# Kernel tuning notes

Measured on AMD Instinct MI355X. Metric: run time of the kernel, lower is better.

The kernel has to match this reference:

```python
import jax, jax.numpy as jnp
import numpy as np
import math

N, E, MUL = 10000, 160000, 128
D = MUL * 4  # 128x0e (128) + 128x1o (384) = 512
NEURONS = 32
EDGE_ATTR_DIM = 32
WEIGHT_NUMEL = 4 * MUL  # 4 uvu tensor-product paths, 128 weights each


def ssp(x):
    return jax.nn.softplus(x) - math.log(2.0)


def irrep_linear(x, W0, b0, W1):
    # o3.Linear on 128x0e+128x1o: mixes mul channels within each irrep, fan-in normalized,
    # bias only on scalar (0e) block.
    s = x[:, :MUL] @ (W0 / jnp.sqrt(MUL)) + b0
    v = x[:, MUL:].reshape(-1, MUL, 3)
    v = jnp.einsum('num,uv->nvm', v, W1) / jnp.sqrt(MUL)
    return jnp.concatenate([s, v.reshape(-1, MUL * 3)], axis=-1)


def inner_product(a, b):
    # InnerProduct: uuu channel-wise irrep inner product, 1/sqrt(dim) normalized
    s = a[:, :MUL] * b[:, :MUL]
    va = a[:, MUL:].reshape(-1, MUL, 3)
    vb = b[:, MUL:].reshape(-1, MUL, 3)
    v = jnp.einsum('num,num->nu', va, vb) / jnp.sqrt(3.0)
    return jnp.concatenate([s, v], axis=-1)


def norm_gate(x, W1, b1, W2, b2):
    # NormGate: per-channel norms of l>0 irreps -> MLP gates -> gate l>0 channels
    v = x[:, MUL:].reshape(-1, MUL, 3)
    norm_v = jnp.sqrt(jnp.sum(v * v, axis=-1) + 1e-12)      # [n, 128]
    f0 = jnp.concatenate([x[:, :MUL], norm_v], axis=-1)     # [n, 256]
    g = jax.nn.silu(f0 @ W1 + b1) @ W2 + b2                 # [n, 256]
    gated = v * g[:, MUL:, None]
    return jnp.concatenate([g[:, :MUL], gated.reshape(-1, MUL * 3)], axis=-1)


def mlp2(x, Wa, Wb):
    # e3nn FullyConnectedNet: fan-in normalized, ssp nonlinearity on hidden layer only
    return ssp(x @ (Wa / jnp.sqrt(Wa.shape[0]))) @ (Wb / jnp.sqrt(Wb.shape[0]))


def setup_inputs():
    key = jax.random.key(0)
    ks = jax.random.split(key, 20)
    r = lambda i, shp: jax.random.normal(ks[i], shp, dtype=jnp.float32)
    return {
        'x': r(0, (N, D)),
        'edge_index': jax.random.randint(ks[1], (2, E), 0, N, dtype=jnp.int32),
        'edge_attr': jax.random.uniform(ks[2], (E, EDGE_ATTR_DIM), dtype=jnp.float32),
        'edge_sh': r(3, (E, 4)),
        'Wp0': r(4, (MUL, MUL)), 'bp0': jnp.zeros((MUL,), jnp.float32), 'Wp1': r(5, (MUL, MUL)),
        'ngW1': r(6, (2 * MUL, 2 * MUL)) / 16.0, 'ngb1': jnp.zeros((2 * MUL,), jnp.float32),
        'ngW2': r(7, (2 * MUL, 2 * MUL)) / 16.0, 'ngb2': jnp.zeros((2 * MUL,), jnp.float32),
        'Wn0': r(8, (MUL, MUL)), 'bn0': jnp.zeros((MUL,), jnp.float32), 'Wn1': r(9, (MUL, MUL)),
        'fcnW1': r(10, (EDGE_ATTR_DIM, NEURONS)), 'fcnW2': r(11, (NEURONS, WEIGHT_NUMEL)),
        'l0W1': r(12, (3 * MUL, NEURONS)), 'l0W2': r(13, (NEURONS, WEIGHT_NUMEL)),
        'Wo0': r(14, (MUL, MUL)), 'bo0': jnp.zeros((MUL,), jnp.float32), 'Wo1': r(15, (MUL, MUL)),
    }


def reference(x, edge_index, edge_attr, edge_sh, Wp0, bp0, Wp1, ngW1, ngb1, ngW2, ngb2,
              Wn0, bn0, Wn1, fcnW1, fcnW2, l0W1, l0W2, Wo0, bo0, Wo1):
    edge_dst, edge_src = edge_index[0], edge_index[1]
    # invariant edge descriptor s0 from pre-linear + inner product
    pre_x = irrep_linear(x, Wp0, bp0, Wp1)
    ip = inner_product(pre_x[edge_dst], pre_x[edge_src])[:, MUL:]             # [E,128]
    s0 = jnp.concatenate([pre_x[edge_dst][:, :MUL], pre_x[edge_src][:, :MUL], ip], axis=-1)  # [E,384]
    # norm-gate + linear on node features
    x = norm_gate(x, ngW1, ngb1, ngW2, ngb2)
    x = irrep_linear(x, Wn0, bn0, Wn1)
    self_x = x
    # per-edge tensor-product weights: fc_node(edge_attr) * layer_l0(s0)
    w = mlp2(edge_attr, fcnW1, fcnW2) * mlp2(s0, l0W1, l0W2)                   # [E,512]
    w1, w2, w3, w4 = w[:, :MUL], w[:, MUL:2 * MUL], w[:, 2 * MUL:3 * MUL], w[:, 3 * MUL:]
    xs = x[edge_src]
    xs0 = xs[:, :MUL]                     # [E,128]
    xs1 = xs[:, MUL:].reshape(E, MUL, 3)  # [E,128,3]
    sh0 = edge_sh[:, 0:1]
    sh1 = edge_sh[:, 1:4]
    # uvu CG tensor product paths: 0ex0e->0e, 0ex1o->1o, 1ox0e->1o, 1ox1o->0e
    c0, c1 = 0.5, jnp.sqrt(3.0) / 2.0  # path norm sqrt(ir_out.dim / n_paths)
    out0 = c0 * (w1 * xs0 * sh0 + w4 * jnp.einsum('eum,em->eu', xs1, sh1) / jnp.sqrt(3.0))
    out1 = c1 * (w2[:, :, None] * xs0[:, :, None] * sh1[:, None, :]
                 + w3[:, :, None] * xs1 * sh0[:, :, None])
    edge_feat = jnp.concatenate([out0, out1.reshape(E, MUL * 3)], axis=-1)     # [E,512]
    # scatter-aggregate to destination nodes, residual, output linear
    out = jax.ops.segment_sum(edge_feat, edge_dst, num_segments=N)
    out = out + self_x
    return irrep_linear(out, Wo0, bo0, Wo1)
```

## Files before the change

### kernel.cpp

```cpp
#include <hip/hip_runtime.h>
#include <hip/hip_fp16.h>
#include <math.h>

#define NN 10000
#define EE 160000
#define DPB 8

#define RS128 0.08838834764831845f
#define RS384 0.05103103630798287f
#define RS32  0.17677669529663687f
#define R3    0.57735026918962576f
#define C1V   0.86602540378443865f

typedef _Float16 half8 __attribute__((ext_vector_type(8)));
typedef float f32x4 __attribute__((ext_vector_type(4)));

__device__ __forceinline__ float sspf(float x) {
    return fmaxf(x, 0.0f) + log1pf(__expf(-fabsf(x))) - 0.69314718055994530942f;
}

__device__ __forceinline__ void packone(const float* __restrict__ W,
                                        _Float16* __restrict__ P,
                                        int K, int N, int off) {
    const int KS = K >> 5;
    int j = off & 7, lane = (off >> 3) & 63, rest = off >> 9;
    int ks = rest % KS, ct = rest / KS;
    int k = ks * 32 + ((lane >> 4) << 3) + j;
    int c = ct * 16 + (lane & 15);
    P[off] = (_Float16)W[k * N + c];
}

__global__ __launch_bounds__(256) void k_packall(
    const float* __restrict__ Wp0, const float* __restrict__ Wp1,
    const float* __restrict__ Wn0, const float* __restrict__ Wn1,
    const float* __restrict__ Wo0, const float* __restrict__ Wo1,
    const float* __restrict__ ngW1, const float* __restrict__ ngW2,
    const float* __restrict__ l0W1, const float* __restrict__ fcnW1,
    const float* __restrict__ fcnW2, const float* __restrict__ l0W2,
    _Float16* __restrict__ pWp0, _Float16* __restrict__ pWp1,
    _Float16* __restrict__ pWn0, _Float16* __restrict__ pWn1,
    _Float16* __restrict__ pWo0, _Float16* __restrict__ pWo1,
    _Float16* __restrict__ png1, _Float16* __restrict__ png2,
    _Float16* __restrict__ pWc, _Float16* __restrict__ pWa,
    _Float16* __restrict__ Wf_t, _Float16* __restrict__ Wl_t) {
    int idx = blockIdx.x * 256 + threadIdx.x;
    if (idx < 98304) {
        int seg = idx >> 14, off = idx & 16383;
        if (seg == 0) packone(Wp0, pWp0, 128, 128, off);
        else if (seg == 1) packone(Wp1, pWp1, 128, 128, off);
        else if (seg == 2) packone(Wn0, pWn0, 128, 128, off);
        else if (seg == 3) packone(Wn1, pWn1, 128, 128, off);
        else if (seg == 4) packone(Wo0, pWo0, 128, 128, off);
        else packone(Wo1, pWo1, 128, 128, off);
    } else if (idx < 229376) {
        int r = idx - 98304;
        if (r < 65536) packone(ngW1, png1, 256, 256, r);
        else packone(ngW2, png2, 256, 256, r - 65536);
    } else if (idx < 233472) {
        packone(l0W1 + 256 * 32, pWc, 128, 32, idx - 229376);
    } else if (idx < 234496) {
        packone(fcnW1, pWa, 32, 32, idx - 233472);
    } else {
        int off = idx - 234496;
        int k = off & 31, c = off >> 5;
        Wf_t[c * 32 + k] = (_Float16)fcnW2[k * 512 + c];
        Wl_t[c * 32 + k] = (_Float16)l0W2[k * 512 + c];
    }
}

__global__ __launch_bounds__(256) void k_irrep_m(
    const float* __restrict__ X, const _Float16* __restrict__ pW0,
    const float* __restrict__ b0, const _Float16* __restrict__ pW1,
    float* __restrict__ out) {
    __shared__ _Float16 Xr[4][16][136];
    const int t = threadIdx.x, lane = t & 63, w = t >> 6;
    const int nb = blockIdx.x * 16;
    for (int idx = t; idx < 16 * 128; idx += 256) {
        int n = idx >> 7, c4 = idx & 127;
        const float4 v = *(const float4*)(X + (size_t)(nb + n) * 512 + 4 * c4);
        float vals[4] = {v.x, v.y, v.z, v.w};
        int c = 4 * c4;
#pragma unroll
        for (int j = 0; j < 4; ++j) {
            int cc = c + j;
            if (cc < 128) Xr[0][n][cc] = (_Float16)vals[j];
            else { int d = cc - 128; Xr[1 + d % 3][n][d / 3] = (_Float16)vals[j]; }
        }
    }
    __syncthreads();
    const _Float16* pW = (w == 0) ? pW0 : pW1;
    const int row16 = lane & 15, kg = lane >> 4;
    f32x4 acc[8];
    const f32x4 zero = {0.0f, 0.0f, 0.0f, 0.0f};
#pragma unroll
    for (int ct = 0; ct < 8; ++ct) acc[ct] = zero;
    for (int ks = 0; ks < 4; ++ks) {
        const half8 a = *(const half8*)&Xr[w][row16][ks * 32 + kg * 8];
#pragma unroll
        for (int ct = 0; ct < 8; ++ct) {
            const half8 b = *(const half8*)(pW + (((ct * 4 + ks) * 64 + lane) << 3));
            acc[ct] = __builtin_amdgcn_mfma_f32_16x16x32_f16(a, b, acc[ct], 0, 0, 0);
        }
    }
#pragma unroll
    for (int ct = 0; ct < 8; ++ct) {
        const int col = ct * 16 + row16;
        const float bb = (w == 0) ? b0[col] : 0.0f;
#pragma unroll
        for (int r = 0; r < 4; ++r) {
            const int node = nb + kg * 4 + r;
            const float val = acc[ct][r] * RS128 + bb;
            if (w == 0) out[(size_t)node * 512 + col] = val;
            else out[(size_t)node * 512 + 128 + 3 * col + (w - 1)] = val;
        }
    }
}

__global__ __launch_bounds__(256) void k_self_m(
    const float* __restrict__ X,
    const _Float16* __restrict__ png1, const float* __restrict__ ngb1,
    const _Float16* __restrict__ png2, const float* __restrict__ ngb2,
    const _Float16* __restrict__ pWn0, const float* __restrict__ bn0,
    const _Float16* __restrict__ pWn1,
    float* __restrict__ selfx) {
    __shared__ _Float16 f0h[16][264];
    __shared__ _Float16 t1h[16][264];
    __shared__ _Float16 xvh[3][16][136];
    const int t = threadIdx.x, lane = t & 63, w = t >> 6;
    const int nb = blockIdx.x * 16;
    const int row16 = lane & 15, kg = lane >> 4;
    const f32x4 zero = {0.0f, 0.0f, 0.0f, 0.0f};

    for (int idx = t; idx < 16 * 128; idx += 256) {
        int n = idx >> 7, c4 = idx & 127;
        const float4 v = *(const float4*)(X + (size_t)(nb + n) * 512 + 4 * c4);
        float vals[4] = {v.x, v.y, v.z, v.w};
        int c = 4 * c4;
#pragma unroll
        for (int j = 0; j < 4; ++j) {
            int cc = c + j;
            if (cc < 128) f0h[n][cc] = (_Float16)vals[j];
            else { int d = cc - 128; xvh[d % 3][n][d / 3] = (_Float16)vals[j]; }
        }
    }
    __syncthreads();
    for (int idx = t; idx < 16 * 128; idx += 256) {
        int n = idx >> 7, u = idx & 127;
        float a = (float)xvh[0][n][u], b = (float)xvh[1][n][u], c = (float)xvh[2][n][u];
        f0h[n][128 + u] = (_Float16)sqrtf(fmaf(a, a, fmaf(b, b, fmaf(c, c, 1e-12f))));
    }
    __syncthreads();
    {
        f32x4 acc[4];
#pragma unroll
        for (int i = 0; i < 4; ++i) acc[i] = zero;
        for (int ks = 0; ks < 8; ++ks) {
            const half8 a = *(const half8*)&f0h[row16][ks * 32 + kg * 8];
#pragma unroll
            for (int c2 = 0; c2 < 4; ++c2) {
                const int ct = 4 * w + c2;
                const half8 b = *(const half8*)(png1 + (((ct * 8 + ks) * 64 + lane) << 3));
                acc[c2] = __builtin_amdgcn_mfma_f32_16x16x32_f16(a, b, acc[c2], 0, 0, 0);
            }
        }
#pragma unroll
        for (int c2 = 0; c2 < 4; ++c2) {
            const int col = (4 * w + c2) * 16 + row16;
            const float bb = ngb1[col];
#pragma unroll
            for (int r = 0; r < 4; ++r) {
                const float z = acc[c2][r] + bb;
                t1h[kg * 4 + r][col] = (_Float16)(z / (1.0f + __expf(-z)));
            }
        }
    }
    __syncthreads();
    {
        f32x4 acc[4];
#pragma unroll
        for (int i = 0; i < 4; ++i) acc[i] = zero;
        for (int ks = 0; ks < 8; ++ks) {
            const half8 a = *(const half8*)&t1h[row16][ks * 32 + kg * 8];
#pragma unroll
            for (int c2 = 0; c2 < 4; ++c2) {
                const int ct = 4 * w + c2;
                const half8 b = *(const half8*)(png2 + (((ct * 8 + ks) * 64 + lane) << 3));
                acc[c2] = __builtin_amdgcn_mfma_f32_16x16x32_f16(a, b, acc[c2], 0, 0, 0);
            }
        }
        __syncthreads();
#pragma unroll
        for (int c2 = 0; c2 < 4; ++c2) {
            const int col = (4 * w + c2) * 16 + row16;
            const float bb = ngb2[col];
#pragma unroll
            for (int r = 0; r < 4; ++r)
                f0h[kg * 4 + r][col] = (_Float16)(acc[c2][r] + bb);
        }
    }
    __syncthreads();
    for (int idx = t; idx < 16 * 128; idx += 256) {
        int n = idx >> 7, u = idx & 127;
        const _Float16 g = f0h[n][128 + u];
        xvh[0][n][u] = xvh[0][n][u] * g;
        xvh[1][n][u] = xvh[1][n][u] * g;
        xvh[2][n][u] = xvh[2][n][u] * g;
    }
    __syncthreads();
    {
        const _Float16* pw = (w == 0) ? pWn0 : pWn1;
        f32x4 acc[8];
#pragma unroll
        for (int ct = 0; ct < 8; ++ct) acc[ct] = zero;
        for (int ks = 0; ks < 4; ++ks) {
            const half8 a = (w == 0)
                ? *(const half8*)&f0h[row16][ks * 32 + kg * 8]
                : *(const half8*)&xvh[w - 1][row16][ks * 32 + kg * 8];
#pragma unroll
            for (int ct = 0; ct < 8; ++ct) {
                const half8 b = *(const half8*)(pw + (((ct * 4 + ks) * 64 + lane) << 3));
                acc[ct] = __builtin_amdgcn_mfma_f32_16x16x32_f16(a, b, acc[ct], 0, 0, 0);
            }
        }
#pragma unroll
        for (int ct = 0; ct < 8; ++ct) {
            const int col = ct * 16 + row16;
            const float bb = (w == 0) ? bn0[col] : 0.0f;
#pragma unroll
            for (int r = 0; r < 4; ++r) {
                const int node = nb + kg * 4 + r;
                const float val = acc[ct][r] * RS128 + bb;
                if (w == 0) selfx[(size_t)node * 512 + col] = val;
                else selfx[(size_t)node * 512 + 128 + 3 * col + (w - 1)] = val;
            }
        }
    }
}

__global__ __launch_bounds__(256) void k_pre(
    const float* __restrict__ prex, const float* __restrict__ l0W1,
    float* __restrict__ pAB) {
    __shared__ float xs[8][128];
    const int t = threadIdx.x;
    const int nb = blockIdx.x * 8;
    for (int idx = t; idx < 8 * 128; idx += 256) {
        int n = idx >> 7, u = idx & 127;
        xs[n][u] = prex[(size_t)(nb + n) * 512 + u];
    }
    __syncthreads();
    const int n = t >> 5, k = t & 31;
    float a = 0, b = 0;
    for (int u = 0; u < 128; ++u) {
        float s = xs[n][u];
        a = fmaf(s, l0W1[u * 32 + k], a);
        b = fmaf(s, l0W1[(128 + u) * 32 + k], b);
    }
    pAB[(size_t)(nb + n) * 64 + k] = a;
    pAB[(size_t)(nb + n) * 64 + 32 + k] = b;
}

__global__ __launch_bounds__(256) void k_deg(const int* __restrict__ ei, int* __restrict__ deg) {
    int e = blockIdx.x * 256 + threadIdx.x;
    if (e < EE) atomicAdd(&deg[ei[e]], 1);
}

__global__ __launch_bounds__(1024) void k_scan(const int* __restrict__ deg, int* __restrict__ row_ptr) {
    __shared__ int part[1024];
    const int t = threadIdx.x;
    const int base = t * 10;
    int loc[10];
    int s = 0;
#pragma unroll
    for (int i = 0; i < 10; ++i) {
        int idx = base + i;
        int d = (idx < NN) ? deg[idx] : 0;
        loc[i] = s;
        s += d;
    }
    part[t] = s;
    __syncthreads();
    for (int off = 1; off < 1024; off <<= 1) {
        int v = (t >= off) ? part[t - off] : 0;
        __syncthreads();
        part[t] += v;
        __syncthreads();
    }
    int excl = (t > 0) ? part[t - 1] : 0;
#pragma unroll
    for (int i = 0; i < 10; ++i) {
        int idx = base + i;
        if (idx <= NN) row_ptr[idx] = excl + loc[i];
    }
}

__global__ __launch_bounds__(256) void k_fill(const int* __restrict__ ei,
                                              const int* __restrict__ row_ptr,
                                              int* __restrict__ cursor,
                                              int* __restrict__ csr_eid) {
    int e = blockIdx.x * 256 + threadIdx.x;
    if (e < EE) {
        int d = ei[e];
        int pos = atomicAdd(&cursor[d], 1);
        csr_eid[row_ptr[d] + pos] = e;
    }
}

__global__ __launch_bounds__(256) void k_hidden_m(
    const float* __restrict__ prex, const float* __restrict__ pAB,
    const int* __restrict__ edge_index, const float* __restrict__ edge_attr,
    const int* __restrict__ csr_eid,
    const _Float16* __restrict__ pWc, const _Float16* __restrict__ pWa,
    __half* __restrict__ hh) {
    const int pb = blockIdx.x * 32;
    const int t = threadIdx.x, lane = t & 63, w = t >> 6;
    __shared__ _Float16 ipl[32][132];
    __shared__ _Float16 eal[32][36];
    __shared__ _Float16 h1o[32][32];
    __shared__ _Float16 hao[32][32];
    __shared__ int dsts[32], srcs[32], eids[32];

    if (t < 32) {
        const int id = csr_eid[pb + t];
        eids[t] = id;
        dsts[t] = edge_index[id];
        srcs[t] = edge_index[EE + id];
    }
    __syncthreads();
    for (int idx = t; idx < 32 * 32; idx += 256) {
        int e = idx >> 5, j = idx & 31;
        eal[e][j] = (_Float16)edge_attr[(size_t)eids[e] * 32 + j];
    }
    for (int idx = t; idx < 32 * 128; idx += 256) {
        int e = idx >> 7, u = idx & 127;
        const float* pd = prex + (size_t)dsts[e] * 512 + 128 + 3 * u;
        const float* ps = prex + (size_t)srcs[e] * 512 + 128 + 3 * u;
        ipl[e][u] = (_Float16)((pd[0] * ps[0] + pd[1] * ps[1] + pd[2] * ps[2]) * R3);
    }
    __syncthreads();

    const int row16 = lane & 15, kg = lane >> 4;
    const int mt = w >> 1, ct = w & 1;
    const int e0 = mt * 16;
    const f32x4 zero = {0.0f, 0.0f, 0.0f, 0.0f};
    const int kc = ct * 16 + row16;

    {
        f32x4 acc = zero;
#pragma unroll
        for (int ks = 0; ks < 4; ++ks) {
            const half8 a = *(const half8*)&ipl[e0 + row16][ks * 32 + kg * 8];
            const half8 b = *(const half8*)(pWc + (((ct * 4 + ks) * 64 + lane) << 3));
            acc = __builtin_amdgcn_mfma_f32_16x16x32_f16(a, b, acc, 0, 0, 0);
        }
#pragma unroll
        for (int r = 0; r < 4; ++r) {
            const int e = e0 + kg * 4 + r;
            const float v = acc[r] + pAB[(size_t)dsts[e] * 64 + kc]
                                   + pAB[(size_t)srcs[e] * 64 + 32 + kc];
            h1o[e][kc] = (_Float16)sspf(v * RS384);
        }
    }
    {
        const half8 a = *(const half8*)&eal[e0 + row16][kg * 8];
        const half8 b = *(const half8*)(pWa + ((ct * 64 + lane) << 3));
        f32x4 acc = __builtin_amdgcn_mfma_f32_16x16x32_f16(a, b, zero, 0, 0, 0);
#pragma unroll
        for (int r = 0; r < 4; ++r) {
            const int e = e0 + kg * 4 + r;
            hao[e][kc] = (_Float16)sspf((float)acc[r] * RS32);
        }
    }
    __syncthreads();
    for (int idx = t; idx < 32 * 32; idx += 256) {
        const int e = idx >> 5, j = idx & 31;
        unsigned vv;
        if (j < 16) {
            __half2 h2 = __halves2half2((__half)h1o[e][2 * j], (__half)h1o[e][2 * j + 1]);
            vv = *(unsigned*)&h2;
        } else {
            const int jj = j - 16;
            __half2 h2 = __halves2half2((__half)hao[e][2 * jj], (__half)hao[e][2 * jj + 1]);
            vv = *(unsigned*)&h2;
        }
        ((unsigned*)hh)[(size_t)(pb + e) * 32 + j] = vv;
    }
}

__global__ __launch_bounds__(512) void k_accum(
    const __half* __restrict__ hh, const float* __restrict__ selfx,
    const int* __restrict__ edge_index, const float* __restrict__ edge_sh,
    const int* __restrict__ row_ptr, const int* __restrict__ csr_eid,
    const _Float16* __restrict__ Wf_t, const _Float16* __restrict__ Wl_t,
    float* __restrict__ outacc) {
    const int dst0 = blockIdx.x * DPB;
    const int t = threadIdx.x;
    const int lane = t & 63;
    const int wid = t >> 6;
    const int lcol = lane & 15;
    const int kg = lane >> 4;
    const int u = 16 * wid + lcol;
    const int koff = kg * 8;

    __shared__ __align__(16) _Float16 h1s[2][4][16][8];
    __shared__ __align__(16) _Float16 has[2][4][16][8];
    __shared__ float shl[2][16][4];
    __shared__ int srcs[2][16];
    __shared__ int cbeg[DPB], cne[DPB], cchk[DPB + 1];

    if (t < DPB) {
        const int b = row_ptr[dst0 + t];
        cbeg[t] = b;
        cne[t] = row_ptr[dst0 + t + 1] - b;
    }
    __syncthreads();
    if (t == 0) {
        int s = 0;
#pragma unroll
        for (int i = 0; i < DPB; ++i) { cchk[i] = s; s += max(1, (cne[i] + 15) >> 4); }
        cchk[DPB] = s;
    }
    half8 bf[4], bl[4];
#pragma unroll
    for (int q = 0; q < 4; ++q) {
        const int col = q * 128 + u;
        bf[q] = *(const half8*)(Wf_t + col * 32 + koff);
        bl[q] = *(const half8*)(Wl_t + col * 32 + koff);
    }
    __syncthreads();
    const int nc = cchk[DPB];
    const float inv32 = 1.0f / 32.0f;

    float acc0 = 0, acc1 = 0, acc2 = 0, acc3 = 0;

    unsigned rhh = 0;
    int rsrc = 0;
    float4 rsh = {0.0f, 0.0f, 0.0f, 0.0f};

    const int se = t >> 5, sw = t & 31;

    auto issue = [&](int ci) {
        int dd = 0;
        while (dd + 1 < DPB && ci >= cchk[dd + 1]) ++dd;
        const int c0 = (ci - cchk[dd]) << 4;
        const int ce = min(16, cne[dd] - c0);
        const int pos = cbeg[dd] + c0;
        rhh = (se < ce) ? ((const unsigned*)hh)[(size_t)(pos + se) * 32 + sw] : 0u;
        if (t < 16) {
            if (t < ce) {
                const int id = csr_eid[pos + t];
                rsrc = edge_index[EE + id];
                rsh = *(const float4*)(edge_sh + (size_t)id * 4);
            } else {
                rsrc = 0;
                rsh = make_float4(0.0f, 0.0f, 0.0f, 0.0f);
            }
        }
    };

    auto flush = [&](int dd) {
        acc0 += __shfl_xor(acc0, 16, 64); acc0 += __shfl_xor(acc0, 32, 64);
        acc1 += __shfl_xor(acc1, 16, 64); acc1 += __shfl_xor(acc1, 32, 64);
        acc2 += __shfl_xor(acc2, 16, 64); acc2 += __shfl_xor(acc2, 32, 64);
        acc3 += __shfl_xor(acc3, 16, 64); acc3 += __shfl_xor(acc3, 32, 64);
        if (lane < 16) {
            const size_t g = (size_t)(dst0 + dd) * 512;
            outacc[g + u] = acc0 + selfx[g + u];
            outacc[g + 128 + 3 * u + 0] = acc1 + selfx[g + 128 + 3 * u + 0];
            outacc[g + 128 + 3 * u + 1] = acc2 + selfx[g + 128 + 3 * u + 1];
            outacc[g + 128 + 3 * u + 2] = acc3 + selfx[g + 128 + 3 * u + 2];
        }
        acc0 = acc1 = acc2 = acc3 = 0;
    };

    issue(0);
    int cur = 0, cur_dd = 0;
    for (int ci = 0; ci < nc; ++ci) {
        if (sw < 16) ((unsigned*)h1s[cur])[(sw >> 2) * 64 + se * 4 + (sw & 3)] = rhh;
        else         ((unsigned*)has[cur])[((sw - 16) >> 2) * 64 + se * 4 + ((sw - 16) & 3)] = rhh;
        if (t < 16) {
            srcs[cur][t] = rsrc;
            shl[cur][t][0] = rsh.x; shl[cur][t][1] = rsh.y;
            shl[cur][t][2] = rsh.z; shl[cur][t][3] = rsh.w;
        }
        int dd = 0;
        while (dd + 1 < DPB && ci >= cchk[dd + 1]) ++dd;
        const int c0 = (ci - cchk[dd]) << 4;
        const int ce = min(16, cne[dd] - c0);
        if (ci + 1 < nc) issue(ci + 1);
        __syncthreads();
        if (dd != cur_dd) { flush(cur_dd); cur_dd = dd; }

        const half8 haf = *(const half8*)(&has[cur][kg][lcol][0]);
        const half8 h1f = *(const half8*)(&h1s[cur][kg][lcol][0]);
        const f32x4 zero = {0.0f, 0.0f, 0.0f, 0.0f};
        f32x4 A[4], B[4];
#pragma unroll
        for (int q = 0; q < 4; ++q) {
            A[q] = __builtin_amdgcn_mfma_f32_16x16x32_f16(haf, bf[q], zero, 0, 0, 0);
            B[q] = __builtin_amdgcn_mfma_f32_16x16x32_f16(h1f, bl[q], zero, 0, 0, 0);
        }
#pragma unroll
        for (int r = 0; r < 4; ++r) {
            const int e = kg * 4 + r;
            if (e < ce) {
                const float w1 = A[0][r] * B[0][r] * inv32;
                const float w2 = A[1][r] * B[1][r] * inv32;
                const float w3 = A[2][r] * B[2][r] * inv32;
                const float w4 = A[3][r] * B[3][r] * inv32;
                const int src = srcs[cur][e];
                const float sh0 = shl[cur][e][0], s1x = shl[cur][e][1];
                const float s1y = shl[cur][e][2], s1z = shl[cur][e][3];
                const float* sr = selfx + (size_t)src * 512;
                const float xs0 = sr[u];
                const float* sv = sr + 128 + 3 * u;
                const float xv0 = sv[0], xv1 = sv[1], xv2 = sv[2];
                const float dv = xv0 * s1x + xv1 * s1y + xv2 * s1z;
                acc0 += 0.5f * (w1 * xs0 * sh0 + w4 * dv * R3);
                acc1 += C1V * (w2 * xs0 * s1x + w3 * xv0 * sh0);
                acc2 += C1V * (w2 * xs0 * s1y + w3 * xv1 * sh0);
                acc3 += C1V * (w2 * xs0 * s1z + w3 * xv2 * sh0);
            }
        }
        cur ^= 1;
    }
    flush(cur_dd);
}

extern "C" void kernel_launch(void* const* d_in, const int* in_sizes, int n_in,
                              void* d_out, int out_size, void* d_ws, size_t ws_size,
                              hipStream_t stream) {
    const float* x = (const float*)d_in[0];
    const int* edge_index = (const int*)d_in[1];
    const float* edge_attr = (const float*)d_in[2];
    const float* edge_sh = (const float*)d_in[3];
    const float* Wp0 = (const float*)d_in[4];
    const float* bp0 = (const float*)d_in[5];
    const float* Wp1 = (const float*)d_in[6];
    const float* ngW1 = (const float*)d_in[7];
    const float* ngb1 = (const float*)d_in[8];
    const float* ngW2 = (const float*)d_in[9];
    const float* ngb2 = (const float*)d_in[10];
    const float* Wn0 = (const float*)d_in[11];
    const float* bn0 = (const float*)d_in[12];
    const float* Wn1 = (const float*)d_in[13];
    const float* fcnW1 = (const float*)d_in[14];
    const float* fcnW2 = (const float*)d_in[15];
    const float* l0W1 = (const float*)d_in[16];
    const float* l0W2 = (const float*)d_in[17];
    const float* Wo0 = (const float*)d_in[18];
    const float* bo0 = (const float*)d_in[19];
    const float* Wo1 = (const float*)d_in[20];

    float* out = (float*)d_out;
    float* prex = out;
    float* selfx = (float*)d_ws;
    int* deg = (int*)(selfx + (size_t)NN * 512);
    int* cursor = deg + NN;
    int* row_ptr = cursor + NN;
    int* csr_eid = row_ptr + NN + 1;
    float* pAB = (float*)(csr_eid + EE);
    __half* hh = (__half*)(pAB + (size_t)NN * 64);
    _Float16* Wf_t = (_Float16*)(hh + (size_t)EE * 64);
    _Float16* Wl_t = Wf_t + 512 * 32;
    _Float16* pWp0 = Wl_t + 512 * 32;
    _Float16* pWp1 = pWp0 + 128 * 128;
    _Float16* pWn0 = pWp1 + 128 * 128;
    _Float16* pWn1 = pWn0 + 128 * 128;
    _Float16* pWo0 = pWn1 + 128 * 128;
    _Float16* pWo1 = pWo0 + 128 * 128;
    _Float16* png1 = pWo1 + 128 * 128;
    _Float16* png2 = png1 + 256 * 256;
    _Float16* pWc  = png2 + 256 * 256;
    _Float16* pWa  = pWc + 128 * 32;

    hipMemsetAsync(deg, 0, 2 * NN * sizeof(int), stream);

    k_packall<<<980, 256, 0, stream>>>(Wp0, Wp1, Wn0, Wn1, Wo0, Wo1, ngW1, ngW2,
                                       l0W1, fcnW1, fcnW2, l0W2,
                                       pWp0, pWp1, pWn0, pWn1, pWo0, pWo1,
                                       png1, png2, pWc, pWa, Wf_t, Wl_t);

    k_irrep_m<<<NN / 16, 256, 0, stream>>>(x, pWp0, bp0, pWp1, prex);
    k_pre<<<NN / 8, 256, 0, stream>>>(prex, l0W1, pAB);
    k_self_m<<<NN / 16, 256, 0, stream>>>(x, ngW1 ? png1 : png1, ngb1, png2, ngb2, pWn0, bn0, pWn1, selfx);
    k_deg<<<EE / 256, 256, 0, stream>>>(edge_index, deg);
    k_scan<<<1, 1024, 0, stream>>>(deg, row_ptr);
    k_fill<<<EE / 256, 256, 0, stream>>>(edge_index, row_ptr, cursor, csr_eid);
    k_hidden_m<<<EE / 32, 256, 0, stream>>>(prex, pAB, edge_index, edge_attr, csr_eid,
                                            pWc, pWa, hh);
    k_accum<<<NN / DPB, 512, 0, stream>>>(hh, selfx, edge_index, edge_sh, row_ptr, csr_eid,
                                          Wf_t, Wl_t, out);
    k_irrep_m<<<NN / 16, 256, 0, stream>>>(out, pWo0, bo0, pWo1, out);
}
```

Baseline: 262.3 us.

## Store self features as interleaved fp16 and prefetch gathered source rows

The self-interaction output is now stored in fp16 with the four irrep components of each channel packed contiguously (half4 per channel), staged through shared memory before writing. The accumulation kernel gathers each source node's half4 with a single 8-byte load, and it issues that load for the next chunk while the current one is computed, instead of making four scattered fp32 loads inside the compute loop. This halves gather bandwidth and hides the gather latency. It adds fp16 rounding of the residual and message inputs and more registers per thread.

```diff
diff --git a/kernel.cpp b/kernel.cpp
--- a/kernel.cpp
+++ b/kernel.cpp
@@ -13,6 +13,7 @@
 #define C1V   0.86602540378443865f
 
 typedef _Float16 half8 __attribute__((ext_vector_type(8)));
+typedef _Float16 half4 __attribute__((ext_vector_type(4)));
 typedef float f32x4 __attribute__((ext_vector_type(4)));
 
 __device__ __forceinline__ float sspf(float x) {
@@ -122,7 +123,7 @@
     const _Float16* __restrict__ png2, const float* __restrict__ ngb2,
     const _Float16* __restrict__ pWn0, const float* __restrict__ bn0,
     const _Float16* __restrict__ pWn1,
-    float* __restrict__ selfx) {
+    _Float16* __restrict__ selfx_h) {
     __shared__ _Float16 f0h[16][264];
     __shared__ _Float16 t1h[16][264];
     __shared__ _Float16 xvh[3][16][136];
@@ -228,12 +229,18 @@
             const float bb = (w == 0) ? bn0[col] : 0.0f;
 #pragma unroll
             for (int r = 0; r < 4; ++r) {
-                const int node = nb + kg * 4 + r;
+                const int n = kg * 4 + r;
                 const float val = acc[ct][r] * RS128 + bb;
-                if (w == 0) selfx[(size_t)node * 512 + col] = val;
-                else selfx[(size_t)node * 512 + 128 + 3 * col + (w - 1)] = val;
+                if (w == 0) f0h[n][col] = (_Float16)val;
+                else xvh[w - 1][n][col] = (_Float16)val;
             }
         }
+    }
+    __syncthreads();
+    for (int idx = t; idx < 16 * 128; idx += 256) {
+        int n = idx >> 7, u = idx & 127;
+        half4 sx = {f0h[n][u], xvh[0][n][u], xvh[1][n][u], xvh[2][n][u]};
+        *(half4*)(selfx_h + (size_t)(nb + n) * 512 + (u << 2)) = sx;
     }
 }
 
@@ -387,7 +394,7 @@
 }
 
 __global__ __launch_bounds__(512) void k_accum(
-    const __half* __restrict__ hh, const float* __restrict__ selfx,
+    const __half* __restrict__ hh, const _Float16* __restrict__ selfx_h,
     const int* __restrict__ edge_index, const float* __restrict__ edge_sh,
     const int* __restrict__ row_ptr, const int* __restrict__ csr_eid,
     const _Float16* __restrict__ Wf_t, const _Float16* __restrict__ Wl_t,
@@ -404,7 +411,6 @@
     __shared__ __align__(16) _Float16 h1s[2][4][16][8];
     __shared__ __align__(16) _Float16 has[2][4][16][8];
     __shared__ float shl[2][16][4];
-    __shared__ int srcs[2][16];
     __shared__ int cbeg[DPB], cne[DPB], cchk[DPB + 1];
 
     if (t < DPB) {
@@ -433,8 +439,10 @@
     float acc0 = 0, acc1 = 0, acc2 = 0, acc3 = 0;
 
     unsigned rhh = 0;
-    int rsrc = 0;
     float4 rsh = {0.0f, 0.0f, 0.0f, 0.0f};
+    const half4 h4z = {(_Float16)0, (_Float16)0, (_Float16)0, (_Float16)0};
+    half4 nsx[4] = {h4z, h4z, h4z, h4z};
+    half4 csx[4];
 
     const int se = t >> 5, sw = t & 31;
 
@@ -448,11 +456,20 @@
         if (t < 16) {
             if (t < ce) {
                 const int id = csr_eid[pos + t];
-                rsrc = edge_index[EE + id];
                 rsh = *(const float4*)(edge_sh + (size_t)id * 4);
             } else {
-                rsrc = 0;
                 rsh = make_float4(0.0f, 0.0f, 0.0f, 0.0f);
+            }
+        }
+#pragma unroll
+        for (int r = 0; r < 4; ++r) {
+            const int e = kg * 4 + r;
+            if (e < ce) {
+                const int id2 = csr_eid[pos + e];
+                const int s = edge_index[EE + id2];
+                nsx[r] = *(const half4*)(selfx_h + (size_t)s * 512 + (u << 2));
+            } else {
+                nsx[r] = h4z;
             }
         }
     };
@@ -464,10 +481,11 @@
         acc3 += __shfl_xor(acc3, 16, 64); acc3 += __shfl_xor(acc3, 32, 64);
         if (lane < 16) {
             const size_t g = (size_t)(dst0 + dd) * 512;
-            outacc[g + u] = acc0 + selfx[g + u];
-            outacc[g + 128 + 3 * u + 0] = acc1 + selfx[g + 128 + 3 * u + 0];
-            outacc[g + 128 + 3 * u + 1] = acc2 + selfx[g + 128 + 3 * u + 1];
-            outacc[g + 128 + 3 * u + 2] = acc3 + selfx[g + 128 + 3 * u + 2];
+            const half4 sx = *(const half4*)(selfx_h + g + (u << 2));
+            outacc[g + u] = acc0 + (float)sx.x;
+            outacc[g + 128 + 3 * u + 0] = acc1 + (float)sx.y;
+            outacc[g + 128 + 3 * u + 1] = acc2 + (float)sx.z;
+            outacc[g + 128 + 3 * u + 2] = acc3 + (float)sx.w;
         }
         acc0 = acc1 = acc2 = acc3 = 0;
     };
@@ -478,14 +496,13 @@
         if (sw < 16) ((unsigned*)h1s[cur])[(sw >> 2) * 64 + se * 4 + (sw & 3)] = rhh;
         else         ((unsigned*)has[cur])[((sw - 16) >> 2) * 64 + se * 4 + ((sw - 16) & 3)] = rhh;
         if (t < 16) {
-            srcs[cur][t] = rsrc;
             shl[cur][t][0] = rsh.x; shl[cur][t][1] = rsh.y;
             shl[cur][t][2] = rsh.z; shl[cur][t][3] = rsh.w;
         }
+#pragma unroll
+        for (int r = 0; r < 4; ++r) csx[r] = nsx[r];
         int dd = 0;
         while (dd + 1 < DPB && ci >= cchk[dd + 1]) ++dd;
-        const int c0 = (ci - cchk[dd]) << 4;
-        const int ce = min(16, cne[dd] - c0);
         if (ci + 1 < nc) issue(ci + 1);
         __syncthreads();
         if (dd != cur_dd) { flush(cur_dd); cur_dd = dd; }
@@ -502,24 +519,21 @@
 #pragma unroll
         for (int r = 0; r < 4; ++r) {
             const int e = kg * 4 + r;
-            if (e < ce) {
-                const float w1 = A[0][r] * B[0][r] * inv32;
-                const float w2 = A[1][r] * B[1][r] * inv32;
-                const float w3 = A[2][r] * B[2][r] * inv32;
-                const float w4 = A[3][r] * B[3][r] * inv32;
-                const int src = srcs[cur][e];
-                const float sh0 = shl[cur][e][0], s1x = shl[cur][e][1];
-                const float s1y = shl[cur][e][2], s1z = shl[cur][e][3];
-                const float* sr = selfx + (size_t)src * 512;
-                const float xs0 = sr[u];
-                const float* sv = sr + 128 + 3 * u;
-                const float xv0 = sv[0], xv1 = sv[1], xv2 = sv[2];
-                const float dv = xv0 * s1x + xv1 * s1y + xv2 * s1z;
-                acc0 += 0.5f * (w1 * xs0 * sh0 + w4 * dv * R3);
-                acc1 += C1V * (w2 * xs0 * s1x + w3 * xv0 * sh0);
-                acc2 += C1V * (w2 * xs0 * s1y + w3 * xv1 * sh0);
-                acc3 += C1V * (w2 * xs0 * s1z + w3 * xv2 * sh0);
-            }
+            const float w1 = A[0][r] * B[0][r] * inv32;
+            const float w2 = A[1][r] * B[1][r] * inv32;
+            const float w3 = A[2][r] * B[2][r] * inv32;
+            const float w4 = A[3][r] * B[3][r] * inv32;
+            const float sh0 = shl[cur][e][0], s1x = shl[cur][e][1];
+            const float s1y = shl[cur][e][2], s1z = shl[cur][e][3];
+            const float xs0 = (float)csx[r].x;
+            const float xv0 = (float)csx[r].y;
+            const float xv1 = (float)csx[r].z;
+            const float xv2 = (float)csx[r].w;
+            const float dv = xv0 * s1x + xv1 * s1y + xv2 * s1z;
+            acc0 += 0.5f * (w1 * xs0 * sh0 + w4 * dv * R3);
+            acc1 += C1V * (w2 * xs0 * s1x + w3 * xv0 * sh0);
+            acc2 += C1V * (w2 * xs0 * s1y + w3 * xv1 * sh0);
+            acc3 += C1V * (w2 * xs0 * s1z + w3 * xv2 * sh0);
         }
         cur ^= 1;
     }
@@ -553,8 +567,8 @@
 
     float* out = (float*)d_out;
     float* prex = out;
-    float* selfx = (float*)d_ws;
-    int* deg = (int*)(selfx + (size_t)NN * 512);
+    _Float16* selfx_h = (_Float16*)d_ws;
+    int* deg = (int*)(selfx_h + (size_t)NN * 512);
     int* cursor = deg + NN;
     int* row_ptr = cursor + NN;
     int* csr_eid = row_ptr + NN + 1;
@@ -582,13 +596,14 @@
 
     k_irrep_m<<<NN / 16, 256, 0, stream>>>(x, pWp0, bp0, pWp1, prex);
     k_pre<<<NN / 8, 256, 0, stream>>>(prex, l0W1, pAB);
-    k_self_m<<<NN / 16, 256, 0, stream>>>(x, ngW1 ? png1 : png1, ngb1, png2, ngb2, pWn0, bn0, pWn1, selfx);
+    k_self_m<<<NN / 16, 256, 0, stream>>>(x, png1, ngb1, png2, ngb2, pWn0, bn0, pWn1,
+                                          selfx_h);
     k_deg<<<EE / 256, 256, 0, stream>>>(edge_index, deg);
     k_scan<<<1, 1024, 0, stream>>>(deg, row_ptr);
     k_fill<<<EE / 256, 256, 0, stream>>>(edge_index, row_ptr, cursor, csr_eid);
     k_hidden_m<<<EE / 32, 256, 0, stream>>>(prex, pAB, edge_index, edge_attr, csr_eid,
                                             pWc, pWa, hh);
-    k_accum<<<NN / DPB, 512, 0, stream>>>(hh, selfx, edge_index, edge_sh, row_ptr, csr_eid,
+    k_accum<<<NN / DPB, 512, 0, stream>>>(hh, selfx_h, edge_index, edge_sh, row_ptr, csr_eid,
                                           Wf_t, Wl_t, out);
     k_irrep_m<<<NN / 16, 256, 0, stream>>>(out, pWo0, bo0, pWo1, out);
 }
```

Measured after the change: 299.4 us. 1.14x slower.
